# Kernel tuning notes

Measured on AMD Instinct MI355X. Metric: run time of the kernel, lower is better.

Reference implementation:

```python
import jax, jax.numpy as jnp
import numpy as np

VOCAB = 65
H = 128
L = 8
OUT = 65
B, T = 64, 512


def setup_inputs() -> dict:
    key = jax.random.key(0)
    ks = jax.random.split(key, 8)
    s = 1.0 / np.sqrt(H)
    return {
        "x": jax.random.randint(ks[0], (B, T), 0, VOCAB, dtype=jnp.int32),
        "embed": jax.random.normal(ks[1], (VOCAB, H), dtype=jnp.float32),
        "w_ih": jax.random.uniform(ks[2], (L, H, 4 * H), jnp.float32, -s, s),
        "b_ih": jax.random.uniform(ks[3], (L, 4 * H), jnp.float32, -s, s),
        "w_hh": jax.random.uniform(ks[4], (L, H, 4 * H), jnp.float32, -s, s),
        "b_hh": jax.random.uniform(ks[5], (L, 4 * H), jnp.float32, -s, s),
        "w_out": jax.random.uniform(ks[6], (H, OUT), jnp.float32, -s, s),
        "b_out": jax.random.uniform(ks[7], (OUT,), jnp.float32, -s, s),
    }


def reference(x, embed, w_ih, b_ih, w_hh, b_hh, w_out, b_out):
    xe = embed[x]                     # [B, T, H]
    xe_t = jnp.swapaxes(xe, 0, 1)     # [T, B, H] for scan over time
    h0 = jnp.zeros((L, x.shape[0], H), xe.dtype)
    c0 = jnp.zeros((L, x.shape[0], H), xe.dtype)

    def step(carry, xt):
        hs, cs = carry                # each [L, B, H]
        inp = xt
        new_h, new_c = [], []
        for l in range(L):
            gates = inp @ w_ih[l] + b_ih[l] + hs[l] @ w_hh[l] + b_hh[l]
            i, f, g, o = jnp.split(gates, 4, axis=-1)
            i = jax.nn.sigmoid(i)
            f = jax.nn.sigmoid(f)
            g = jnp.tanh(g)
            o = jax.nn.sigmoid(o)
            c = f * cs[l] + i * g
            h = o * jnp.tanh(c)
            new_h.append(h)
            new_c.append(c)
            inp = h
        out_t = inp @ w_out + b_out   # [B, OUT]
        return (jnp.stack(new_h), jnp.stack(new_c)), out_t

    (hT, cT), outs = jax.lax.scan(step, (h0, c0), xe_t)
    outputs = jnp.swapaxes(outs, 0, 1)  # [B, T, OUT]
    return outputs, (hT, cT)
```

## Files before the change

### kernel.cpp

```cpp
#include <hip/hip_runtime.h>
#include <hip/hip_bf16.h>


#define T_ 512
#define L_ 8
#define H_ 128
#define G4_ 512
#define OUT_ 65
#define B_ 64
#define NG_ 4
#define BG_ 16
#define LDSW_ 136
#define HT_OFF_ (B_ * T_ * OUT_)
#define CT_OFF_ (HT_OFF_ + L_ * B_ * H_)
#define STEP_U64_ 512

typedef __bf16 bf16_t;
typedef bf16_t bf16x8 __attribute__((ext_vector_type(8)));
typedef bf16_t bf16x4 __attribute__((ext_vector_type(4)));
typedef float f32x4 __attribute__((ext_vector_type(4)));
typedef unsigned long long u64;

union U128 { uint4 u; bf16x8 b; };

__device__ __forceinline__ float rcpf(float x) { return __builtin_amdgcn_rcpf(x); }
__device__ __forceinline__ float sigm(float x) { return rcpf(1.f + __expf(-x)); }
__device__ __forceinline__ float tanh_fast(float x) {
  const float e = __expf(-2.f * fabsf(x));
  const float r = 2.f * rcpf(1.f + e) - 1.f;
  return copysignf(r, x);
}
__device__ __forceinline__ int flag_ld(int* p) {
  return __hip_atomic_load(p, __ATOMIC_RELAXED, __HIP_MEMORY_SCOPE_AGENT);
}
__device__ __forceinline__ void flag_st(int* p, int v) {
  __hip_atomic_store(p, v, __ATOMIC_RELAXED, __HIP_MEMORY_SCOPE_AGENT);
}
__device__ __forceinline__ u64 ring_ld(const u64* p) {
  return __hip_atomic_load(const_cast<u64*>(p), __ATOMIC_RELAXED, __HIP_MEMORY_SCOPE_AGENT);
}
__device__ __forceinline__ void ring_st(u64* p, u64 v) {
  __hip_atomic_store(p, v, __ATOMIC_RELAXED, __HIP_MEMORY_SCOPE_AGENT);
}

__global__ void zero_flags(int* flags) { flags[blockIdx.x * 1024 + threadIdx.x] = 0; }

template <int CT, int RING_T>
__global__ __launch_bounds__(512, 2)
void lstm_pipe(const int* __restrict__ xids, const float* __restrict__ embed,
               const float* __restrict__ wih_g, const float* __restrict__ bih_g,
               const float* __restrict__ whh_g, const float* __restrict__ bhh_g,
               const float* __restrict__ wout_g, const float* __restrict__ bout_g,
               float* __restrict__ out, int* __restrict__ flags,
               u64* __restrict__ ring) {
  static_assert(RING_T >= 2 * CT || RING_T >= T_, "need >=2 chunks of ring slack");
  constexpr int NCH = T_ / CT;
  const int l    = blockIdx.x >> 2;
  const int g    = blockIdx.x & 3;
  const int tid  = threadIdx.x;
  const int wv   = tid >> 6;
  const int lane = tid & 63;
  const int q    = lane >> 4;
  const int col  = lane & 15;

  __shared__ __align__(16) bf16_t xchunk[CT][16 * LDSW_];
  __shared__ __align__(16) bf16_t hist[CT][16 * LDSW_];
  __shared__ uint4 wout_lds[5][4][64];

  U128 wih[4][4], whh[4][4];
#pragma unroll
  for (int c = 0; c < 4; ++c) {
    const int n = wv * 16 + c * 128 + col;
#pragma unroll
    for (int kt = 0; kt < 4; ++kt) {
      U128 a, b;
#pragma unroll
      for (int jj = 0; jj < 8; ++jj) {
        const int k = kt * 32 + q * 8 + jj;
        a.b[jj] = (bf16_t)wih_g[(l * H_ + k) * G4_ + n];
        b.b[jj] = (bf16_t)whh_g[(l * H_ + k) * G4_ + n];
      }
      wih[c][kt] = a;
      whh[c][kt] = b;
    }
  }
#pragma unroll
  for (int c = 0; c < 4; ++c)
#pragma unroll
    for (int kt = 0; kt < 4; ++kt) {
      asm volatile("" : "+v"(wih[c][kt].u.x), "+v"(wih[c][kt].u.y),
                        "+v"(wih[c][kt].u.z), "+v"(wih[c][kt].u.w));
      asm volatile("" : "+v"(whh[c][kt].u.x), "+v"(whh[c][kt].u.y),
                        "+v"(whh[c][kt].u.z), "+v"(whh[c][kt].u.w));
    }

  float bias[4];
#pragma unroll
  for (int c = 0; c < 4; ++c) {
    const int n = wv * 16 + c * 128 + col;
    bias[c] = bih_g[l * G4_ + n] + bhh_g[l * G4_ + n];
  }
  float bo = 0.f;
  const bool has_out = (l == L_ - 1) && (wv < 5);
  if (has_out) {
    const int n = wv * 16 + col;
#pragma unroll
    for (int kt = 0; kt < 4; ++kt) {
      U128 w;
#pragma unroll
      for (int jj = 0; jj < 8; ++jj) {
        const int k = kt * 32 + q * 8 + jj;
        w.b[jj] = (n < OUT_) ? (bf16_t)wout_g[k * OUT_ + n] : (bf16_t)(0.f);
      }
      wout_lds[wv][kt][lane] = w.u;
    }
    if (n < OUT_) bo = bout_g[n];
  }

  int* myprod   = flags + ((l * NG_ + g) << 5);
  int* prevprod = (l > 0) ? flags + (((l - 1) * NG_ + g) << 5) : flags;
  int* mycons   = flags + 1024 + ((l * NG_ + g) << 5);
  int* nextcons = (l < L_ - 1) ? flags + 1024 + (((l + 1) * NG_ + g) << 5) : flags;
  u64* myring  = (l < L_ - 1) ? ring + (size_t)(l * NG_ + g) * RING_T * STEP_U64_ : ring;
  const u64* srcring = (l > 0) ? ring + (size_t)((l - 1) * NG_ + g) * RING_T * STEP_U64_ : ring;

  const int aoff = col * LDSW_ + q * 8;
  float cst[4] = {0.f, 0.f, 0.f, 0.f};
  int seen_prod = 0, seen_cons = 0;

  for (int i = tid; i < 16 * LDSW_; i += 512) hist[CT - 1][i] = (bf16_t)(0.f);
  if (l == 0) {
    const int m  = tid >> 5;
    const int c4 = (tid & 31) << 2;
#pragma unroll
    for (int tl = 0; tl < CT; ++tl) {
      const int token = xids[(g * BG_ + m) * T_ + tl];
      const float4 e = *(const float4*)(embed + token * H_ + c4);
      bf16x4 v;
      v[0] = (bf16_t)e.x; v[1] = (bf16_t)e.y; v[2] = (bf16_t)e.z; v[3] = (bf16_t)e.w;
      *(bf16x4*)(&xchunk[tl][m * LDSW_ + c4]) = v;
    }
  } else {
    if (tid == 0) {
      int v;
      do { v = flag_ld(prevprod); } while (v < CT);
      seen_prod = v;
    }
    __syncthreads();
    const int idx = tid >> 2;
    if (idx < CT * 16) {
      const int tl = idx >> 4, m = idx & 15, seg = tid & 3;
      const u64* src = srcring + (size_t)(tl & (RING_T - 1)) * STEP_U64_ + m * 32 + seg * 8;
      u64* dst = (u64*)(&xchunk[tl][m * LDSW_ + seg * 32]);
#pragma unroll
      for (int j = 0; j < 8; ++j) dst[j] = ring_ld(src + j);
    }
  }
  __syncthreads();

#pragma unroll 1
  for (int ch = 0; ch < NCH; ++ch) {
    const int t0 = ch * CT;

    f32x4 gx[CT][4];
#pragma unroll
    for (int tl = 0; tl < CT; ++tl) {
      bf16x8 xa[4];
#pragma unroll
      for (int kt = 0; kt < 4; ++kt)
        xa[kt] = *(const bf16x8*)(&xchunk[tl][aoff + kt * 32]);
#pragma unroll
      for (int c = 0; c < 4; ++c) {
        f32x4 a = (f32x4){bias[c], bias[c], bias[c], bias[c]};
#pragma unroll
        for (int kt = 0; kt < 4; ++kt)
          a = __builtin_amdgcn_mfma_f32_16x16x32_bf16(xa[kt], wih[c][kt].b, a, 0, 0, 0);
        gx[tl][c] = a;
      }
    }

#pragma unroll
    for (int tl = 0; tl < CT; ++tl) {
      bf16x8 ha[4];
#pragma unroll
      for (int kt = 0; kt < 4; ++kt)
        ha[kt] = *(const bf16x8*)(&hist[(tl + CT - 1) % CT][aoff + kt * 32]);
#pragma unroll
      for (int c = 0; c < 4; ++c)
#pragma unroll
        for (int kt = 0; kt < 4; ++kt)
          gx[tl][c] = __builtin_amdgcn_mfma_f32_16x16x32_bf16(ha[kt], whh[c][kt].b, gx[tl][c], 0, 0, 0);

      float hv[4];
      bf16_t hb[4];
#pragma unroll
      for (int r = 0; r < 4; ++r) {
        const float iv = sigm(gx[tl][0][r]);
        const float fv = sigm(gx[tl][1][r]);
        const float gv = tanh_fast(gx[tl][2][r]);
        const float ov = sigm(gx[tl][3][r]);
        const float cv = fv * cst[r] + iv * gv;
        cst[r] = cv;
        const float h = ov * tanh_fast(cv);
        hv[r] = h;
        hb[r] = (bf16_t)h;
      }
      {
        const int jc = wv * 16 + col;
#pragma unroll
        for (int r = 0; r < 4; ++r)
          hist[tl][(q * 4 + r) * LDSW_ + jc] = hb[r];
      }
      if (t0 + tl == T_ - 1) {
        const int jc = wv * 16 + col;
#pragma unroll
        for (int r = 0; r < 4; ++r) {
          const int b = g * BG_ + q * 4 + r;
          out[HT_OFF_ + (l * B_ + b) * H_ + jc] = hv[r];
          out[CT_OFF_ + (l * B_ + b) * H_ + jc] = cst[r];
        }
      }
      __syncthreads();

      if (l < L_ - 1) {
        const u64 val = *(const u64*)(&hist[tl][(tid >> 5) * LDSW_ + ((tid & 31) << 2)]);
        ring_st(&myring[(size_t)((t0 + tl) & (RING_T - 1)) * STEP_U64_ + tid], val);
      }
    }

    if (has_out) {
      const int n = wv * 16 + col;
#pragma unroll
      for (int tl = 0; tl < CT; ++tl) {
        f32x4 oacc = (f32x4){0.f, 0.f, 0.f, 0.f};
#pragma unroll
        for (int kt = 0; kt < 4; ++kt) {
          U128 w;
          w.u = wout_lds[wv][kt][lane];
          const bf16x8 a = *(const bf16x8*)(&hist[tl][col * LDSW_ + kt * 32 + q * 8]);
          oacc = __builtin_amdgcn_mfma_f32_16x16x32_bf16(a, w.b, oacc, 0, 0, 0);
        }
        if (n < OUT_) {
#pragma unroll
          for (int r = 0; r < 4; ++r) {
            const int b = g * BG_ + q * 4 + r;
            out[(b * T_ + (t0 + tl)) * OUT_ + n] = oacc[r] + bo;
          }
        }
      }
    }

    if (ch + 1 < NCH) {
      if (tid == 0) {
        if (RING_T < T_ && l > 0) flag_st(mycons, t0 + CT);
        if (l > 0) {
          const int target = t0 + 2 * CT;
          if (seen_prod < target) {
            int v;
            do { v = flag_ld(prevprod); } while (v < target);
            seen_prod = v;
          }
        }
        if (RING_T < T_ && l < L_ - 1 && t0 + 2 * CT > RING_T) {
          const int need = t0 + 2 * CT - RING_T;
          if (seen_cons < need) {
            int v;
            do { v = flag_ld(nextcons); } while (v < need);
            seen_cons = v;
          }
        }
      }
      __syncthreads();
      if (l < L_ - 1 && tid == 0) {
        flag_st(myprod, t0 + CT);
      }
      if (l == 0) {
        const int m  = tid >> 5;
        const int c4 = (tid & 31) << 2;
#pragma unroll
        for (int tl = 0; tl < CT; ++tl) {
          const int token = xids[(g * BG_ + m) * T_ + t0 + CT + tl];
          const float4 e = *(const float4*)(embed + token * H_ + c4);
          bf16x4 v;
          v[0] = (bf16_t)e.x; v[1] = (bf16_t)e.y; v[2] = (bf16_t)e.z; v[3] = (bf16_t)e.w;
          *(bf16x4*)(&xchunk[tl][m * LDSW_ + c4]) = v;
        }
      } else {
        const int idx = tid >> 2;
        if (idx < CT * 16) {
          const int tl = idx >> 4, m = idx & 15, seg = tid & 3;
          const u64* src = srcring + (size_t)((t0 + CT + tl) & (RING_T - 1)) * STEP_U64_ + m * 32 + seg * 8;
          u64* dst = (u64*)(&xchunk[tl][m * LDSW_ + seg * 32]);
#pragma unroll
          for (int j = 0; j < 8; ++j) dst[j] = ring_ld(src + j);
        }
      }
      __syncthreads();
    } else if (l < L_ - 1) {
      __syncthreads();
      if (tid == 0) {
        flag_st(myprod, T_);
      }
    }
  }
}

extern "C" void kernel_launch(void* const* d_in, const int* in_sizes, int n_in,
                              void* d_out, int out_size, void* d_ws, size_t ws_size,
                              hipStream_t stream) {
  (void)in_sizes; (void)n_in; (void)out_size;
  const int*   x     = (const int*)d_in[0];
  const float* embed = (const float*)d_in[1];
  const float* w_ih  = (const float*)d_in[2];
  const float* b_ih  = (const float*)d_in[3];
  const float* w_hh  = (const float*)d_in[4];
  const float* b_hh  = (const float*)d_in[5];
  const float* w_out = (const float*)d_in[6];
  const float* b_out = (const float*)d_in[7];
  float* out = (float*)d_out;

  int* flags = (int*)d_ws;
  u64* ring  = (u64*)((char*)d_ws + 8192);

  hipLaunchKernelGGL(zero_flags, dim3(2), dim3(1024), 0, stream, flags);

  auto need = [&](int ring_t) { return (size_t)8192 + (size_t)28 * ring_t * 4096; };

  if (ws_size >= need(512)) {
    hipLaunchKernelGGL((lstm_pipe<4, 512>), dim3(L_ * NG_), dim3(512), 0, stream,
                       x, embed, w_ih, b_ih, w_hh, b_hh, w_out, b_out, out, flags, ring);
  } else if (ws_size >= need(16)) {
    hipLaunchKernelGGL((lstm_pipe<4, 16>), dim3(L_ * NG_), dim3(512), 0, stream,
                       x, embed, w_ih, b_ih, w_hh, b_hh, w_out, b_out, out, flags, ring);
  } else if (ws_size >= need(8)) {
    hipLaunchKernelGGL((lstm_pipe<4, 8>), dim3(L_ * NG_), dim3(512), 0, stream,
                       x, embed, w_ih, b_ih, w_hh, b_hh, w_out, b_out, out, flags, ring);
  } else {
    hipLaunchKernelGGL((lstm_pipe<2, 4>), dim3(L_ * NG_), dim3(512), 0, stream,
                       x, embed, w_ih, b_ih, w_hh, b_hh, w_out, b_out, out, flags, ring);
  }
}
```

Baseline: 923.4 us.

## Read layer input directly from ring into MFMA registers, batch ring stores per chunk

Layers above the first no longer stage their input chunk from the global ring into LDS. Each lane instead loads its MFMA A-fragment straight from the ring with relaxed atomic loads. Ring stores of hidden states move out of the per-timestep loop and are done in one batch per chunk, just before the producer flag is published. This removes an LDS staging copy and one barrier per chunk. In exchange it issues more scattered global loads inside the compute loop, and it relies on visibility ordering between the batched ring stores and the flag store.

```diff
diff --git a/kernel.cpp b/kernel.cpp
--- a/kernel.cpp
+++ b/kernel.cpp
@@ -21,7 +21,7 @@
 typedef float f32x4 __attribute__((ext_vector_type(4)));
 typedef unsigned long long u64;
 
-union U128 { uint4 u; bf16x8 b; };
+union U128 { uint4 u; bf16x8 b; u64 d[2]; };
 
 __device__ __forceinline__ float rcpf(float x) { return __builtin_amdgcn_rcpf(x); }
 __device__ __forceinline__ float sigm(float x) { return rcpf(1.f + __expf(-x)); }
@@ -146,15 +146,6 @@
       do { v = flag_ld(prevprod); } while (v < CT);
       seen_prod = v;
     }
-    __syncthreads();
-    const int idx = tid >> 2;
-    if (idx < CT * 16) {
-      const int tl = idx >> 4, m = idx & 15, seg = tid & 3;
-      const u64* src = srcring + (size_t)(tl & (RING_T - 1)) * STEP_U64_ + m * 32 + seg * 8;
-      u64* dst = (u64*)(&xchunk[tl][m * LDSW_ + seg * 32]);
-#pragma unroll
-      for (int j = 0; j < 8; ++j) dst[j] = ring_ld(src + j);
-    }
   }
   __syncthreads();
 
@@ -166,9 +157,21 @@
 #pragma unroll
     for (int tl = 0; tl < CT; ++tl) {
       bf16x8 xa[4];
-#pragma unroll
-      for (int kt = 0; kt < 4; ++kt)
-        xa[kt] = *(const bf16x8*)(&xchunk[tl][aoff + kt * 32]);
+      if (l == 0) {
+#pragma unroll
+        for (int kt = 0; kt < 4; ++kt)
+          xa[kt] = *(const bf16x8*)(&xchunk[tl][aoff + kt * 32]);
+      } else {
+        const u64* xsrc = srcring + (size_t)((t0 + tl) & (RING_T - 1)) * STEP_U64_
+                        + (size_t)col * 32 + q * 2;
+#pragma unroll
+        for (int kt = 0; kt < 4; ++kt) {
+          U128 xf;
+          xf.d[0] = ring_ld(xsrc + kt * 8);
+          xf.d[1] = ring_ld(xsrc + kt * 8 + 1);
+          xa[kt] = xf.b;
+        }
+      }
 #pragma unroll
       for (int c = 0; c < 4; ++c) {
         f32x4 a = (f32x4){bias[c], bias[c], bias[c], bias[c]};
@@ -221,11 +224,6 @@
         }
       }
       __syncthreads();
-
-      if (l < L_ - 1) {
-        const u64 val = *(const u64*)(&hist[tl][(tid >> 5) * LDSW_ + ((tid & 31) << 2)]);
-        ring_st(&myring[(size_t)((t0 + tl) & (RING_T - 1)) * STEP_U64_ + tid], val);
-      }
     }
 
     if (has_out) {
@@ -251,6 +249,13 @@
     }
 
     if (ch + 1 < NCH) {
+      if (l < L_ - 1) {
+#pragma unroll
+        for (int tl = 0; tl < CT; ++tl) {
+          const u64 val = *(const u64*)(&hist[tl][(tid >> 5) * LDSW_ + ((tid & 31) << 2)]);
+          ring_st(&myring[(size_t)((t0 + tl) & (RING_T - 1)) * STEP_U64_ + tid], val);
+        }
+      }
       if (tid == 0) {
         if (RING_T < T_ && l > 0) flag_st(mycons, t0 + CT);
         if (l > 0) {
@@ -285,18 +290,14 @@
           v[0] = (bf16_t)e.x; v[1] = (bf16_t)e.y; v[2] = (bf16_t)e.z; v[3] = (bf16_t)e.w;
           *(bf16x4*)(&xchunk[tl][m * LDSW_ + c4]) = v;
         }
-      } else {
-        const int idx = tid >> 2;
-        if (idx < CT * 16) {
-          const int tl = idx >> 4, m = idx & 15, seg = tid & 3;
-          const u64* src = srcring + (size_t)((t0 + CT + tl) & (RING_T - 1)) * STEP_U64_ + m * 32 + seg * 8;
-          u64* dst = (u64*)(&xchunk[tl][m * LDSW_ + seg * 32]);
-#pragma unroll
-          for (int j = 0; j < 8; ++j) dst[j] = ring_ld(src + j);
-        }
-      }
-      __syncthreads();
+        __syncthreads();
+      }
     } else if (l < L_ - 1) {
+#pragma unroll
+      for (int tl = 0; tl < CT; ++tl) {
+        const u64 val = *(const u64*)(&hist[tl][(tid >> 5) * LDSW_ + ((tid & 31) << 2)]);
+        ring_st(&myring[(size_t)((t0 + tl) & (RING_T - 1)) * STEP_U64_ + tid], val);
+      }
       __syncthreads();
       if (tid == 0) {
         flag_st(myprod, T_);
```

Result: slower. 1.469 ms (+59.1%).
